# Kernel optimization log

Hardware: AMD Instinct MI355X
Metric: run time of the kernel (lower is better)

The kernel has to match this reference:

```python
import jax, jax.numpy as jnp
import numpy as np

KMAX = 5                 # number of wrap shifts per side -> K = 2*KMAX+1 = 11
TWO_PI = 2.0 * np.pi
N_MC, M, D = 32, 8192, 16


def setup_inputs() -> dict:
    key = jax.random.key(0)
    k1, k2, k3 = jax.random.split(key, 3)
    eps = jax.random.normal(k1, (N_MC, M, D), dtype=jnp.float32)
    # raw gamma is stored pre-softplus: inv_softplus(1.5) = log(expm1(1.5))
    base = np.float32(np.log(np.expm1(1.5)))
    gamma_raw = base + 0.1 * jax.random.normal(k2, (M, D), dtype=jnp.float32)
    mu = np.float32(TWO_PI) * jax.random.uniform(k3, (M, D), dtype=jnp.float32)
    return {"eps": eps, "gamma_raw": gamma_raw, "mu": mu}


def reference(eps, gamma_raw, mu):
    # diagonal ReLie on the torus T^D
    scale = jax.nn.softplus(gamma_raw)                     # (M, D) per-dim std
    x = eps * scale                                        # rsample, mean 0: (N_MC, M, D)
    # wrapped-normal log density: sum_j log sum_k N(x_j + 2*pi*k; 0, scale_j^2)
    ks = jnp.arange(-KMAX, KMAX + 1, dtype=x.dtype)        # (K,)
    shifted = x[..., None] + jnp.asarray(TWO_PI, x.dtype) * ks   # (N_MC, M, D, K)
    log_norm = -0.5 * jnp.log(jnp.asarray(TWO_PI, x.dtype)) - jnp.log(scale)  # (M, D)
    lp = log_norm[..., None] - 0.5 * jnp.square(shifted / scale[..., None])   # (N_MC, M, D, K)
    lq = jax.nn.logsumexp(lp, axis=-1).sum(axis=-1)        # (N_MC, M)
    # expmap on torus is identity on angles; transform composes with learned mu (group add mod 2*pi)
    g = jnp.mod(x + mu, jnp.asarray(TWO_PI, x.dtype))      # (N_MC, M, D)
    return g, lq
```

## Files before the change

### kernel.cpp

```cpp
#include <hip/hip_runtime.h>
#include <math.h>


namespace {
constexpr int N_MC = 32;
constexpr int M    = 8192;
constexpr int D    = 16;
constexpr float  TWO_PI_F        = 6.28318530717958647692f;
constexpr float  NEG_HALF_LOG2PI = -0.91893853320467274178f;
constexpr float  INV_TWO_PI_F    = 0.15915494309189533577f;
constexpr double TWO_PI_D        = (double)TWO_PI_F;
constexpr double INV_TWO_PI_D    = 1.0 / TWO_PI_D;
}

__global__ __launch_bounds__(256) void relie_kernel(
    const float* __restrict__ eps,
    const float* __restrict__ gamma_raw,
    const float* __restrict__ mu,
    float* __restrict__ out)
{
    const int tid = blockIdx.x * 256 + threadIdx.x;
    if (tid >= N_MC * M) return;
    const int m = tid & (M - 1);

    const float4* __restrict__ e4  = reinterpret_cast<const float4*>(eps       + (size_t)tid * D);
    const float4* __restrict__ g4  = reinterpret_cast<const float4*>(gamma_raw + (size_t)m   * D);
    const float4* __restrict__ mu4 = reinterpret_cast<const float4*>(mu        + (size_t)m   * D);
    float4* __restrict__ og4       = reinterpret_cast<float4*>(out + (size_t)tid * D);
    float* __restrict__ lq_out     = out + (size_t)N_MC * M * D;

    float lq = 0.0f;
    #pragma unroll
    for (int v = 0; v < 4; ++v) {
        const float4 ev = e4[v];
        const float4 gv = g4[v];
        const float4 mv = mu4[v];
        const float el[4] = {ev.x, ev.y, ev.z, ev.w};
        const float gl[4] = {gv.x, gv.y, gv.z, gv.w};
        const float ml[4] = {mv.x, mv.y, mv.z, mv.w};
        float ol[4];
        #pragma unroll
        for (int j = 0; j < 4; ++j) {
            const float e = el[j];
            const float sc   = __logf(1.0f + __expf(gl[j]));
            const float inv  = __builtin_amdgcn_rcpf(sc);
            const float step = TWO_PI_F * inv;

            const float  t   = fmaf(e, sc, ml[j]);
            const double t_d = (double)t;
            const double k   = trunc(t_d * INV_TWO_PI_D);
            double rem = fma(-k, TWO_PI_D, t_d);
            rem = (rem < 0.0)       ? rem + TWO_PI_D : rem;
            rem = (rem >= TWO_PI_D) ? rem - TWO_PI_D : rem;
            ol[j] = (float)rem;

            const float c  = rintf(e * sc * INV_TWO_PI_F);
            const float zc = fmaf(-c, step, e);
            const float zm = zc - step;
            const float zp = zc + step;
            const float qc = 0.5f * zc * zc;
            const float qm = 0.5f * zm * zm;
            const float qp = 0.5f * zp * zp;
            const float s  = 1.0f + __expf(qc - qm) + __expf(qc - qp);
            lq += NEG_HALF_LOG2PI - qc + __logf(s * inv);
        }
        float4 ov; ov.x = ol[0]; ov.y = ol[1]; ov.z = ol[2]; ov.w = ol[3];
        og4[v] = ov;
    }
    lq_out[tid] = lq;
}

extern "C" void kernel_launch(void* const* d_in, const int* in_sizes, int n_in,
                              void* d_out, int out_size, void* d_ws, size_t ws_size,
                              hipStream_t stream) {
    const float* eps       = (const float*)d_in[0];
    const float* gamma_raw = (const float*)d_in[1];
    const float* mu        = (const float*)d_in[2];
    float* out = (float*)d_out;
    const int total = N_MC * M;
    relie_kernel<<<(total + 255) / 256, 256, 0, stream>>>(eps, gamma_raw, mu, out);
}
```

Baseline: 77.74 us.

## Split each row across four threads for coalesced float4 access

Each (n,m) row of 16 elements is now handled by four consecutive threads, each loading and storing a single float4, so adjacent lanes touch adjacent 16-byte chunks and global accesses coalesce. The per-row log density is combined with two xor shuffles, and one lane in each group of four writes it. This gives four times as many threads, each with less work, which adds shuffle overhead but improves memory access patterns and latency hiding.

```diff
diff --git a/kernel.cpp b/kernel.cpp
--- a/kernel.cpp
+++ b/kernel.cpp
@@ -20,54 +20,53 @@
     float* __restrict__ out)
 {
     const int tid = blockIdx.x * 256 + threadIdx.x;
-    if (tid >= N_MC * M) return;
-    const int m = tid & (M - 1);
+    const int nm  = tid >> 2;
+    const int v   = tid & 3;
+    const int m4  = ((nm & (M - 1)) << 2) | v;
 
-    const float4* __restrict__ e4  = reinterpret_cast<const float4*>(eps       + (size_t)tid * D);
-    const float4* __restrict__ g4  = reinterpret_cast<const float4*>(gamma_raw + (size_t)m   * D);
-    const float4* __restrict__ mu4 = reinterpret_cast<const float4*>(mu        + (size_t)m   * D);
-    float4* __restrict__ og4       = reinterpret_cast<float4*>(out + (size_t)tid * D);
-    float* __restrict__ lq_out     = out + (size_t)N_MC * M * D;
+    const float4 ev = reinterpret_cast<const float4*>(eps)[tid];
+    const float4 gv = reinterpret_cast<const float4*>(gamma_raw)[m4];
+    const float4 mv = reinterpret_cast<const float4*>(mu)[m4];
 
+    const float el[4] = {ev.x, ev.y, ev.z, ev.w};
+    const float gl[4] = {gv.x, gv.y, gv.z, gv.w};
+    const float ml[4] = {mv.x, mv.y, mv.z, mv.w};
+    float ol[4];
     float lq = 0.0f;
+
     #pragma unroll
-    for (int v = 0; v < 4; ++v) {
-        const float4 ev = e4[v];
-        const float4 gv = g4[v];
-        const float4 mv = mu4[v];
-        const float el[4] = {ev.x, ev.y, ev.z, ev.w};
-        const float gl[4] = {gv.x, gv.y, gv.z, gv.w};
-        const float ml[4] = {mv.x, mv.y, mv.z, mv.w};
-        float ol[4];
-        #pragma unroll
-        for (int j = 0; j < 4; ++j) {
-            const float e = el[j];
-            const float sc   = __logf(1.0f + __expf(gl[j]));
-            const float inv  = __builtin_amdgcn_rcpf(sc);
-            const float step = TWO_PI_F * inv;
+    for (int j = 0; j < 4; ++j) {
+        const float e = el[j];
+        const float sc   = __logf(1.0f + __expf(gl[j]));
+        const float inv  = __builtin_amdgcn_rcpf(sc);
+        const float step = TWO_PI_F * inv;
 
-            const float  t   = fmaf(e, sc, ml[j]);
-            const double t_d = (double)t;
-            const double k   = trunc(t_d * INV_TWO_PI_D);
-            double rem = fma(-k, TWO_PI_D, t_d);
-            rem = (rem < 0.0)       ? rem + TWO_PI_D : rem;
-            rem = (rem >= TWO_PI_D) ? rem - TWO_PI_D : rem;
-            ol[j] = (float)rem;
+        const float  t   = fmaf(e, sc, ml[j]);
+        const double t_d = (double)t;
+        const double k   = trunc(t_d * INV_TWO_PI_D);
+        double rem = fma(-k, TWO_PI_D, t_d);
+        rem = (rem < 0.0)       ? rem + TWO_PI_D : rem;
+        rem = (rem >= TWO_PI_D) ? rem - TWO_PI_D : rem;
+        ol[j] = (float)rem;
 
-            const float c  = rintf(e * sc * INV_TWO_PI_F);
-            const float zc = fmaf(-c, step, e);
-            const float zm = zc - step;
-            const float zp = zc + step;
-            const float qc = 0.5f * zc * zc;
-            const float qm = 0.5f * zm * zm;
-            const float qp = 0.5f * zp * zp;
-            const float s  = 1.0f + __expf(qc - qm) + __expf(qc - qp);
-            lq += NEG_HALF_LOG2PI - qc + __logf(s * inv);
-        }
-        float4 ov; ov.x = ol[0]; ov.y = ol[1]; ov.z = ol[2]; ov.w = ol[3];
-        og4[v] = ov;
+        const float c  = rintf(e * sc * INV_TWO_PI_F);
+        const float zc = fmaf(-c, step, e);
+        const float zm = zc - step;
+        const float zp = zc + step;
+        const float qc = 0.5f * zc * zc;
+        const float qm = 0.5f * zm * zm;
+        const float qp = 0.5f * zp * zp;
+        const float s  = 1.0f + __expf(qc - qm) + __expf(qc - qp);
+        lq += NEG_HALF_LOG2PI - qc + __logf(s * inv);
     }
-    lq_out[tid] = lq;
+
+    float4 ov; ov.x = ol[0]; ov.y = ol[1]; ov.z = ol[2]; ov.w = ol[3];
+    reinterpret_cast<float4*>(out)[tid] = ov;
+
+    float r = lq + __shfl_xor(lq, 1);
+    r += __shfl_xor(r, 2);
+    if ((threadIdx.x & 3) == 0)
+        out[(size_t)N_MC * M * D + nm] = r;
 }
 
 extern "C" void kernel_launch(void* const* d_in, const int* in_sizes, int n_in,
@@ -77,6 +76,6 @@
     const float* gamma_raw = (const float*)d_in[1];
     const float* mu        = (const float*)d_in[2];
     float* out = (float*)d_out;
-    const int total = N_MC * M;
-    relie_kernel<<<(total + 255) / 256, 256, 0, stream>>>(eps, gamma_raw, mu, out);
+    const int total = N_MC * M * 4;
+    relie_kernel<<<total / 256, 256, 0, stream>>>(eps, gamma_raw, mu, out);
 }
```

After: 76.98 us. No clear change (-1.0%).
